# Kernel optimization log

Hardware: AMD Instinct MI355X
Metric: run time of the kernel (lower is better)

The kernel has to match this reference:

```python
import jax, jax.numpy as jnp
import numpy as np

N = 50000
IN_DIM = 1024
HID = 64
HEADS = 4
OUT_DIM = 128
NEG_SLOPE = 0.2


def setup_inputs() -> dict:
    key = jax.random.key(0)
    ks = jax.random.split(key, 10)
    x = jax.random.normal(ks[0], (N, IN_DIM), dtype=jnp.float32)
    edge_index = jax.random.randint(ks[1], (2, 800000), 0, N, dtype=jnp.int64)
    # GATConv 1: input_dim -> hidden_dim, heads=HEADS, concat=True
    W1 = jax.random.normal(ks[2], (IN_DIM, HEADS * HID), dtype=jnp.float32) * (1.0 / np.sqrt(IN_DIM))
    att_src1 = jax.random.normal(ks[3], (HEADS, HID), dtype=jnp.float32) * 0.1
    att_dst1 = jax.random.normal(ks[4], (HEADS, HID), dtype=jnp.float32) * 0.1
    b1 = jnp.zeros((HEADS * HID,), dtype=jnp.float32)
    # GATConv 2: hidden_dim*heads -> output_dim, heads=1, concat=False
    W2 = jax.random.normal(ks[5], (HEADS * HID, OUT_DIM), dtype=jnp.float32) * (1.0 / np.sqrt(HEADS * HID))
    att_src2 = jax.random.normal(ks[6], (1, OUT_DIM), dtype=jnp.float32) * 0.1
    att_dst2 = jax.random.normal(ks[7], (1, OUT_DIM), dtype=jnp.float32) * 0.1
    b2 = jnp.zeros((OUT_DIM,), dtype=jnp.float32)
    return {"x": x, "edge_index": edge_index, "W1": W1, "att_src1": att_src1,
            "att_dst1": att_dst1, "b1": b1, "W2": W2, "att_src2": att_src2,
            "att_dst2": att_dst2, "b2": b2}


def _gat_conv(x, src, dst, W, a_src, a_dst, b, heads, concat):
    # x: [N, F_in]; src/dst: [E'] (self-loops already included)
    n = x.shape[0]
    h = (x @ W).reshape(n, heads, -1)                 # [N, H, D]
    # per-node attention halves (PyG style)
    alpha_s = jnp.sum(h * a_src[None], axis=-1)       # [N, H]
    alpha_d = jnp.sum(h * a_dst[None], axis=-1)       # [N, H]
    e = jax.nn.leaky_relu(alpha_s[src] + alpha_d[dst], NEG_SLOPE)  # [E', H]
    # segment softmax over incoming edges of each destination node
    m = jax.ops.segment_max(e, dst, num_segments=n)   # [N, H]
    m = jnp.where(jnp.isfinite(m), m, 0.0)
    e = jnp.exp(e - m[dst])
    s = jax.ops.segment_sum(e, dst, num_segments=n)   # [N, H]
    alpha = e / (s[dst] + 1e-16)                      # [E', H]
    out = jax.ops.segment_sum(h[src] * alpha[:, :, None], dst, num_segments=n)  # [N, H, D]
    out = out.reshape(n, -1) if concat else out.mean(axis=1)
    return out + b


def reference(x, edge_index, W1, att_src1, att_dst1, b1, W2, att_src2, att_dst2, b2):
    n = x.shape[0]
    # PyG GATConv default: add self-loops
    loops = jnp.arange(n, dtype=edge_index.dtype)
    src = jnp.concatenate([edge_index[0], loops])
    dst = jnp.concatenate([edge_index[1], loops])
    # dropout layers are identity in eval mode
    h = _gat_conv(x, src, dst, W1, att_src1, att_dst1, b1, HEADS, concat=True)
    h = jax.nn.elu(h)
    out = _gat_conv(h, src, dst, W2, att_src2, att_dst2, b2, 1, concat=False)
    # F.normalize(p=2, dim=-1)
    norm = jnp.maximum(jnp.linalg.norm(out, axis=-1, keepdims=True), 1e-12)
    return out / norm
```

## Files before the change

kernel.cpp:

```cpp
#include <hip/hip_runtime.h>
#include <math.h>

#define NNODES 50000
#define E0 800000
#define ETOT 850000
#define IN_DIM 1024
#define HEADS 4
#define C1 256
#define C2 128
#define NEG_SLOPE 0.2f

typedef short bf16x8 __attribute__((ext_vector_type(8)));
typedef float f32x4 __attribute__((ext_vector_type(4)));
typedef unsigned short ushort_t;

__device__ __forceinline__ void edge_sd(const int* __restrict__ ei, int e, int& s, int& d) {
    if (e < E0) { s = ei[e]; d = ei[E0 + e]; }
    else        { s = e - E0; d = s; }
}

__device__ __forceinline__ ushort_t f2b(float f) {
    unsigned u = __float_as_uint(f);
    return (ushort_t)((u + 0x7fffu + ((u >> 16) & 1u)) >> 16);
}
__device__ __forceinline__ float bf2f(ushort_t u) {
    return __uint_as_float((unsigned)u << 16);
}
__device__ __forceinline__ float lrelu(float v) { return v > 0.f ? v : NEG_SLOPE * v; }

__device__ __forceinline__ bf16x8 cvt_bf8(float4 f0, float4 f1) {
    bf16x8 p;
    p[0] = f2b(f0.x); p[1] = f2b(f0.y); p[2] = f2b(f0.z); p[3] = f2b(f0.w);
    p[4] = f2b(f1.x); p[5] = f2b(f1.y); p[6] = f2b(f1.z); p[7] = f2b(f1.w);
    return p;
}

__global__ __launch_bounds__(256) void wtrans_kernel(const float* __restrict__ W,
                                                     ushort_t* __restrict__ WT,
                                                     int K, int N)
{
    int idx = blockIdx.x * 256 + threadIdx.x;
    if (idx >= K * N) return;
    int k = idx / N, n = idx % N;
    WT[((size_t)(k >> 3) * N + n) * 8 + (k & 7)] = f2b(W[idx]);
}

__global__ __launch_bounds__(256, 3) void gemm_fb(const float* __restrict__ A,
                                                  const ushort_t* __restrict__ Bblk,
                                                  ushort_t* __restrict__ Cb,
                                                  int M, int N, int K)
{
    __shared__ __align__(16) ushort_t As[32 * 64 * 8];

    const int tid  = threadIdx.x;
    const int lane = tid & 63;
    const int wid  = tid >> 6;
    const int wr   = wid >> 1, wc = wid & 1;
    const int rowBase = blockIdx.y * 64;
    const int colBase = blockIdx.x * 128;
    const int r0 = lane & 15;
    const int kh = lane >> 4;

    const int srow = tid >> 2;
    const int sq   = tid & 3;
    const float* aSrc = A + (size_t)min(rowBase + srow, M - 1) * K + sq * 64;
    ushort_t* aDst = As + (sq * 8) * 512 + srow * 8;

    const ushort_t* bBase = Bblk + ((size_t)kh * N + colBase + wc * 64 + r0) * 8;

    const ushort_t* aRd = As + kh * 512 + (wr * 32 + r0) * 8;

    f32x4 zero = {0.f, 0.f, 0.f, 0.f};
    f32x4 acc[2][4];
    #pragma unroll
    for (int i = 0; i < 2; ++i)
        #pragma unroll
        for (int j = 0; j < 4; ++j) acc[i][j] = zero;

    float4 st[16];
    #pragma unroll
    for (int i = 0; i < 16; ++i) st[i] = *(const float4*)(aSrc + i * 4);

    const int nstep = K >> 8;
    for (int s = 0; s < nstep; ++s) {
        __syncthreads();
        #pragma unroll
        for (int j = 0; j < 8; ++j)
            *(bf16x8*)(aDst + j * 512) = cvt_bf8(st[2 * j], st[2 * j + 1]);
        __syncthreads();

        if (s + 1 < nstep) {
            const float* nsrc = aSrc + (size_t)(s + 1) * 256;
            #pragma unroll
            for (int i = 0; i < 16; ++i) st[i] = *(const float4*)(nsrc + i * 4);
        }

        #pragma unroll
        for (int j = 0; j < 8; ++j) {
            const ushort_t* bit = bBase + ((size_t)(s * 32 + j * 4) * N) * 8;
            bf16x8 bF[4];
            #pragma unroll
            for (int fj = 0; fj < 4; ++fj)
                bF[fj] = *(const bf16x8*)(bit + (size_t)fj * 128);
            bf16x8 aF0 = *(const bf16x8*)(aRd + j * 2048);
            bf16x8 aF1 = *(const bf16x8*)(aRd + j * 2048 + 128);
            #pragma unroll
            for (int fj = 0; fj < 4; ++fj) {
                acc[0][fj] = __builtin_amdgcn_mfma_f32_16x16x32_bf16(aF0, bF[fj], acc[0][fj], 0, 0, 0);
                acc[1][fj] = __builtin_amdgcn_mfma_f32_16x16x32_bf16(aF1, bF[fj], acc[1][fj], 0, 0, 0);
            }
        }
    }

    #pragma unroll
    for (int fi = 0; fi < 2; ++fi) {
        int row0 = rowBase + wr * 32 + fi * 16 + kh * 4;
        #pragma unroll
        for (int i = 0; i < 4; ++i) {
            int row = row0 + i;
            if (row < M) {
                #pragma unroll
                for (int fj = 0; fj < 4; ++fj)
                    Cb[(size_t)row * N + colBase + wc * 64 + fj * 16 + r0] = f2b(acc[fi][fj][i]);
            }
        }
    }
}

__global__ __launch_bounds__(256, 4) void gemm_bb(const ushort_t* __restrict__ Ab,
                                                  const ushort_t* __restrict__ Bblk,
                                                  ushort_t* __restrict__ Cb,
                                                  int M, int N, int K)
{
    __shared__ __align__(16) ushort_t As[32 * 64 * 8];

    const int tid  = threadIdx.x;
    const int lane = tid & 63;
    const int wid  = tid >> 6;
    const int wr   = wid >> 1, wc = wid & 1;
    const int rowBase = blockIdx.y * 64;
    const int colBase = blockIdx.x * 128;
    const int r0 = lane & 15;
    const int kh = lane >> 4;

    const int srow = tid >> 2;
    const int sq   = tid & 3;
    const ushort_t* aSrc = Ab + (size_t)min(rowBase + srow, M - 1) * K + sq * 64;
    ushort_t* aDst = As + (sq * 8) * 512 + srow * 8;

    const ushort_t* bBase = Bblk + ((size_t)kh * N + colBase + wc * 64 + r0) * 8;
    const ushort_t* aRd = As + kh * 512 + (wr * 32 + r0) * 8;

    f32x4 zero = {0.f, 0.f, 0.f, 0.f};
    f32x4 acc[2][4];
    #pragma unroll
    for (int i = 0; i < 2; ++i)
        #pragma unroll
        for (int j = 0; j < 4; ++j) acc[i][j] = zero;

    bf16x8 st[8];
    #pragma unroll
    for (int j = 0; j < 8; ++j) st[j] = *(const bf16x8*)(aSrc + j * 8);

    const int nstep = K >> 8;
    for (int s = 0; s < nstep; ++s) {
        __syncthreads();
        #pragma unroll
        for (int j = 0; j < 8; ++j)
            *(bf16x8*)(aDst + j * 512) = st[j];
        __syncthreads();

        if (s + 1 < nstep) {
            const ushort_t* nsrc = aSrc + (size_t)(s + 1) * 256;
            #pragma unroll
            for (int j = 0; j < 8; ++j) st[j] = *(const bf16x8*)(nsrc + j * 8);
        }

        #pragma unroll
        for (int j = 0; j < 8; ++j) {
            const ushort_t* bit = bBase + ((size_t)(s * 32 + j * 4) * N) * 8;
            bf16x8 bF[4];
            #pragma unroll
            for (int fj = 0; fj < 4; ++fj)
                bF[fj] = *(const bf16x8*)(bit + (size_t)fj * 128);
            bf16x8 aF0 = *(const bf16x8*)(aRd + j * 2048);
            bf16x8 aF1 = *(const bf16x8*)(aRd + j * 2048 + 128);
            #pragma unroll
            for (int fj = 0; fj < 4; ++fj) {
                acc[0][fj] = __builtin_amdgcn_mfma_f32_16x16x32_bf16(aF0, bF[fj], acc[0][fj], 0, 0, 0);
                acc[1][fj] = __builtin_amdgcn_mfma_f32_16x16x32_bf16(aF1, bF[fj], acc[1][fj], 0, 0, 0);
            }
        }
    }

    #pragma unroll
    for (int fi = 0; fi < 2; ++fi) {
        int row0 = rowBase + wr * 32 + fi * 16 + kh * 4;
        #pragma unroll
        for (int i = 0; i < 4; ++i) {
            int row = row0 + i;
            if (row < M) {
                #pragma unroll
                for (int fj = 0; fj < 4; ++fj)
                    Cb[(size_t)row * N + colBase + wc * 64 + fj * 16 + r0] = f2b(acc[fi][fj][i]);
            }
        }
    }
}

__global__ __launch_bounds__(256) void alpha1_kernel(const ushort_t* __restrict__ h1b,
                                                     const float* __restrict__ asrc,
                                                     const float* __restrict__ adst,
                                                     float* __restrict__ out_s,
                                                     float* __restrict__ out_d)
{
    int n = blockIdx.x;
    int t = threadIdx.x;
    float h = bf2f(h1b[(size_t)n * C1 + t]);
    float s = h * asrc[t];
    float d = h * adst[t];
    #pragma unroll
    for (int off = 32; off > 0; off >>= 1) {
        s += __shfl_down(s, off);
        d += __shfl_down(d, off);
    }
    if ((t & 63) == 0) {
        out_s[n * HEADS + (t >> 6)] = s;
        out_d[n * HEADS + (t >> 6)] = d;
    }
}

__global__ __launch_bounds__(64) void alpha2_kernel(const ushort_t* __restrict__ h2b,
                                                    const float* __restrict__ asrc,
                                                    const float* __restrict__ adst,
                                                    float* __restrict__ out_s,
                                                    float* __restrict__ out_d)
{
    int n = blockIdx.x;
    int t = threadIdx.x;
    float a = bf2f(h2b[(size_t)n * C2 + t]);
    float b = bf2f(h2b[(size_t)n * C2 + t + 64]);
    float s = a * asrc[t] + b * asrc[t + 64];
    float d = a * adst[t] + b * adst[t + 64];
    #pragma unroll
    for (int off = 32; off > 0; off >>= 1) {
        s += __shfl_down(s, off);
        d += __shfl_down(d, off);
    }
    if (t == 0) { out_s[n] = s; out_d[n] = d; }
}

__global__ __launch_bounds__(256) void deg_kernel(const int* __restrict__ ei,
                                                  int* __restrict__ deg)
{
    int e = blockIdx.x * blockDim.x + threadIdx.x;
    if (e >= ETOT) return;
    int s, d; edge_sd(ei, e, s, d);
    atomicAdd(&deg[d], 1);
}

#define SCAN_T 1024
__global__ __launch_bounds__(SCAN_T) void scan_kernel(const int* __restrict__ deg,
                                                      int* __restrict__ rowptr)
{
    __shared__ int wsum[16];
    __shared__ int chunk_tot;
    __shared__ int carry_s;
    const int t = threadIdx.x, lane = t & 63, w = t >> 6;
    if (t == 0) carry_s = 0;
    __syncthreads();
    for (int base = 0; base < NNODES; base += SCAN_T * 4) {
        int idx = base + t * 4;
        int v0 = (idx + 0 < NNODES) ? deg[idx + 0] : 0;
        int v1 = (idx + 1 < NNODES) ? deg[idx + 1] : 0;
        int v2 = (idx + 2 < NNODES) ? deg[idx + 2] : 0;
        int v3 = (idx + 3 < NNODES) ? deg[idx + 3] : 0;
        int p0 = v0, p1 = p0 + v1, p2 = p1 + v2, p3 = p2 + v3;
        int incl = p3;
        #pragma unroll
        for (int off = 1; off < 64; off <<= 1) {
            int nb = __shfl_up(incl, off);
            if (lane >= off) incl += nb;
        }
        if (lane == 63) wsum[w] = incl;
        __syncthreads();
        if (w == 0 && lane < 16) {
            int ws = wsum[lane];
            int wincl = ws;
            #pragma unroll
            for (int off = 1; off < 16; off <<= 1) {
                int nb = __shfl_up(wincl, off);
                if (lane >= off) wincl += nb;
            }
            wsum[lane] = wincl - ws;
            if (lane == 15) chunk_tot = wincl;
        }
        __syncthreads();
        int carry = carry_s;
        int basev = carry + wsum[w] + (incl - p3);
        if (idx + 0 < NNODES) rowptr[idx + 0] = basev;
        if (idx + 1 < NNODES) rowptr[idx + 1] = basev + p0;
        if (idx + 2 < NNODES) rowptr[idx + 2] = basev + p1;
        if (idx + 3 < NNODES) rowptr[idx + 3] = basev + p2;
        __syncthreads();
        if (t == 0) carry_s = carry + chunk_tot;
        __syncthreads();
    }
    if (threadIdx.x == 0) rowptr[NNODES] = carry_s;
}

__global__ __launch_bounds__(256) void scatter_kernel(const int* __restrict__ ei,
                                                      int* __restrict__ cursor,
                                                      int* __restrict__ srcs)
{
    int e = blockIdx.x * blockDim.x + threadIdx.x;
    if (e >= ETOT) return;
    int s, d; edge_sd(ei, e, s, d);
    int pos = atomicAdd(&cursor[d], 1);
    srcs[pos] = s;
}

__global__ __launch_bounds__(256) void weights1_kernel(const int* __restrict__ rowptr,
                                                       const int* __restrict__ srcs,
                                                       const float4* __restrict__ as1,
                                                       const float4* __restrict__ ad1,
                                                       float4* __restrict__ wbuf)
{
    int d = blockIdx.x * 4 + (threadIdx.x >> 6);
    if (d >= NNODES) return;
    int lane = threadIdx.x & 63;
    int beg = rowptr[d], end = rowptr[d + 1];
    float4 adv = ad1[d];
    float m0 = -INFINITY, m1 = -INFINITY, m2 = -INFINITY, m3 = -INFINITY;
    for (int i = beg + lane; i < end; i += 64) {
        int s = srcs[i];
        float4 av = as1[s];
        m0 = fmaxf(m0, lrelu(av.x + adv.x));
        m1 = fmaxf(m1, lrelu(av.y + adv.y));
        m2 = fmaxf(m2, lrelu(av.z + adv.z));
        m3 = fmaxf(m3, lrelu(av.w + adv.w));
    }
    #pragma unroll
    for (int off = 32; off > 0; off >>= 1) {
        m0 = fmaxf(m0, __shfl_xor(m0, off));
        m1 = fmaxf(m1, __shfl_xor(m1, off));
        m2 = fmaxf(m2, __shfl_xor(m2, off));
        m3 = fmaxf(m3, __shfl_xor(m3, off));
    }
    float s0 = 0.f, s1 = 0.f, s2 = 0.f, s3 = 0.f;
    for (int i = beg + lane; i < end; i += 64) {
        int s = srcs[i];
        float4 av = as1[s];
        float w0 = expf(lrelu(av.x + adv.x) - m0);
        float w1 = expf(lrelu(av.y + adv.y) - m1);
        float w2 = expf(lrelu(av.z + adv.z) - m2);
        float w3 = expf(lrelu(av.w + adv.w) - m3);
        wbuf[i] = make_float4(w0, w1, w2, w3);
        s0 += w0; s1 += w1; s2 += w2; s3 += w3;
    }
    #pragma unroll
    for (int off = 32; off > 0; off >>= 1) {
        s0 += __shfl_xor(s0, off);
        s1 += __shfl_xor(s1, off);
        s2 += __shfl_xor(s2, off);
        s3 += __shfl_xor(s3, off);
    }
    float i0 = 1.f / (s0 + 1e-16f), i1 = 1.f / (s1 + 1e-16f);
    float i2 = 1.f / (s2 + 1e-16f), i3 = 1.f / (s3 + 1e-16f);
    for (int i = beg + lane; i < end; i += 64) {
        float4 wv = wbuf[i];
        wbuf[i] = make_float4(wv.x * i0, wv.y * i1, wv.z * i2, wv.w * i3);
    }
}

__global__ __launch_bounds__(256) void weights2_kernel(const int* __restrict__ rowptr,
                                                       const int* __restrict__ srcs,
                                                       const float* __restrict__ as2,
                                                       const float* __restrict__ ad2,
                                                       float* __restrict__ wbuf)
{
    int d = blockIdx.x * 4 + (threadIdx.x >> 6);
    if (d >= NNODES) return;
    int lane = threadIdx.x & 63;
    int beg = rowptr[d], end = rowptr[d + 1];
    float adv = ad2[d];
    float m = -INFINITY;
    for (int i = beg + lane; i < end; i += 64)
        m = fmaxf(m, lrelu(as2[srcs[i]] + adv));
    #pragma unroll
    for (int off = 32; off > 0; off >>= 1) m = fmaxf(m, __shfl_xor(m, off));
    float sm = 0.f;
    for (int i = beg + lane; i < end; i += 64) {
        float w = expf(lrelu(as2[srcs[i]] + adv) - m);
        wbuf[i] = w;
        sm += w;
    }
    #pragma unroll
    for (int off = 32; off > 0; off >>= 1) sm += __shfl_xor(sm, off);
    float inv = 1.f / (sm + 1e-16f);
    for (int i = beg + lane; i < end; i += 64) wbuf[i] *= inv;
}

__global__ __launch_bounds__(256) void aggr1_csr(const int* __restrict__ rowptr,
                                                 const int* __restrict__ srcs,
                                                 const ushort_t* __restrict__ h1b,
                                                 const float* __restrict__ wbuf,
                                                 const float* __restrict__ b1,
                                                 ushort_t* __restrict__ out)
{
    int d = blockIdx.x * 4 + (threadIdx.x >> 6);
    if (d >= NNODES) return;
    int lane = threadIdx.x & 63;
    int c0 = lane * 4;
    int head = lane >> 4;
    int beg = rowptr[d], end = rowptr[d + 1];
    float a0 = 0.f, a1 = 0.f, a2 = 0.f, a3 = 0.f;
    int i = beg;
    for (; i + 3 < end; i += 4) {
        int s0 = srcs[i], s1 = srcs[i + 1], s2 = srcs[i + 2], s3 = srcs[i + 3];
        float w0 = wbuf[i * 4 + head],     w1 = wbuf[i * 4 + 4 + head];
        float w2 = wbuf[i * 4 + 8 + head], w3 = wbuf[i * 4 + 12 + head];
        ushort4 v0 = *(const ushort4*)(h1b + (size_t)s0 * C1 + c0);
        ushort4 v1 = *(const ushort4*)(h1b + (size_t)s1 * C1 + c0);
        ushort4 v2 = *(const ushort4*)(h1b + (size_t)s2 * C1 + c0);
        ushort4 v3 = *(const ushort4*)(h1b + (size_t)s3 * C1 + c0);
        a0 = fmaf(w0, bf2f(v0.x), a0); a1 = fmaf(w0, bf2f(v0.y), a1);
        a2 = fmaf(w0, bf2f(v0.z), a2); a3 = fmaf(w0, bf2f(v0.w), a3);
        a0 = fmaf(w1, bf2f(v1.x), a0); a1 = fmaf(w1, bf2f(v1.y), a1);
        a2 = fmaf(w1, bf2f(v1.z), a2); a3 = fmaf(w1, bf2f(v1.w), a3);
        a0 = fmaf(w2, bf2f(v2.x), a0); a1 = fmaf(w2, bf2f(v2.y), a1);
        a2 = fmaf(w2, bf2f(v2.z), a2); a3 = fmaf(w2, bf2f(v2.w), a3);
        a0 = fmaf(w3, bf2f(v3.x), a0); a1 = fmaf(w3, bf2f(v3.y), a1);
        a2 = fmaf(w3, bf2f(v3.z), a2); a3 = fmaf(w3, bf2f(v3.w), a3);
    }
    for (; i < end; ++i) {
        int s0 = srcs[i];
        float w0 = wbuf[i * 4 + head];
        ushort4 v0 = *(const ushort4*)(h1b + (size_t)s0 * C1 + c0);
        a0 = fmaf(w0, bf2f(v0.x), a0); a1 = fmaf(w0, bf2f(v0.y), a1);
        a2 = fmaf(w0, bf2f(v0.z), a2); a3 = fmaf(w0, bf2f(v0.w), a3);
    }
    float4 bv = *(const float4*)(b1 + c0);
    float o0 = a0 + bv.x, o1 = a1 + bv.y, o2 = a2 + bv.z, o3 = a3 + bv.w;
    ushort4 r;
    r.x = f2b(o0 > 0.f ? o0 : (expf(o0) - 1.f));
    r.y = f2b(o1 > 0.f ? o1 : (expf(o1) - 1.f));
    r.z = f2b(o2 > 0.f ? o2 : (expf(o2) - 1.f));
    r.w = f2b(o3 > 0.f ? o3 : (expf(o3) - 1.f));
    *(ushort4*)(out + (size_t)d * C1 + c0) = r;
}

__global__ __launch_bounds__(256) void aggr2_csr(const int* __restrict__ rowptr,
                                                 const int* __restrict__ srcs,
                                                 const ushort_t* __restrict__ h2b,
                                                 const float* __restrict__ wbuf,
                                                 const float* __restrict__ b2,
                                                 float* __restrict__ out)
{
    int d = blockIdx.x * 4 + (threadIdx.x >> 6);
    if (d >= NNODES) return;
    int lane = threadIdx.x & 63;
    int c0 = lane * 2;
    int beg = rowptr[d], end = rowptr[d + 1];
    float a0 = 0.f, a1 = 0.f;
    int i = beg;
    for (; i + 3 < end; i += 4) {
        int s0 = srcs[i], s1 = srcs[i + 1], s2 = srcs[i + 2], s3 = srcs[i + 3];
        float w0 = wbuf[i], w1 = wbuf[i + 1], w2 = wbuf[i + 2], w3 = wbuf[i + 3];
        ushort2 v0 = *(const ushort2*)(h2b + (size_t)s0 * C2 + c0);
        ushort2 v1 = *(const ushort2*)(h2b + (size_t)s1 * C2 + c0);
        ushort2 v2 = *(const ushort2*)(h2b + (size_t)s2 * C2 + c0);
        ushort2 v3 = *(const ushort2*)(h2b + (size_t)s3 * C2 + c0);
        a0 = fmaf(w0, bf2f(v0.x), a0); a1 = fmaf(w0, bf2f(v0.y), a1);
        a0 = fmaf(w1, bf2f(v1.x), a0); a1 = fmaf(w1, bf2f(v1.y), a1);
        a0 = fmaf(w2, bf2f(v2.x), a0); a1 = fmaf(w2, bf2f(v2.y), a1);
        a0 = fmaf(w3, bf2f(v3.x), a0); a1 = fmaf(w3, bf2f(v3.y), a1);
    }
    for (; i < end; ++i) {
        float w0 = wbuf[i];
        ushort2 v0 = *(const ushort2*)(h2b + (size_t)srcs[i] * C2 + c0);
        a0 = fmaf(w0, bf2f(v0.x), a0); a1 = fmaf(w0, bf2f(v0.y), a1);
    }
    float2 bv = *(const float2*)(b2 + c0);
    float o0 = a0 + bv.x, o1 = a1 + bv.y;
    float sq = o0 * o0 + o1 * o1;
    #pragma unroll
    for (int off = 32; off > 0; off >>= 1) sq += __shfl_xor(sq, off);
    float inv = 1.0f / fmaxf(sqrtf(sq), 1e-12f);
    float2 r = make_float2(o0 * inv, o1 * inv);
    *(float2*)(out + (size_t)d * C2 + c0) = r;
}

extern "C" void kernel_launch(void* const* d_in, const int* in_sizes, int n_in,
                              void* d_out, int out_size, void* d_ws, size_t ws_size,
                              hipStream_t stream)
{
    const float* x     = (const float*)d_in[0];
    const int*   ei    = (const int*)d_in[1];
    const float* W1    = (const float*)d_in[2];
    const float* asrc1 = (const float*)d_in[3];
    const float* adst1 = (const float*)d_in[4];
    const float* b1    = (const float*)d_in[5];
    const float* W2    = (const float*)d_in[6];
    const float* asrc2 = (const float*)d_in[7];
    const float* adst2 = (const float*)d_in[8];
    const float* b2    = (const float*)d_in[9];
    float* out = (float*)d_out;

    char* ws = (char*)d_ws;
    size_t off = 0;
    auto alloc = [&](size_t nbytes) {
        void* p = ws + off;
        off += (nbytes + 15) & ~(size_t)15;
        return p;
    };
    ushort_t* h1b    = (ushort_t*)alloc((size_t)NNODES * C1 * 2);
    ushort_t* act1b  = (ushort_t*)alloc((size_t)NNODES * C1 * 2);
    ushort_t* h2b    = (ushort_t*)alloc((size_t)NNODES * C2 * 2);
    ushort_t* W1blk  = (ushort_t*)alloc((size_t)C1 * IN_DIM * 2);
    ushort_t* W2blk  = (ushort_t*)alloc((size_t)C2 * C1 * 2);
    float*    as1    = (float*)alloc((size_t)NNODES * HEADS * 4);
    float*    ad1    = (float*)alloc((size_t)NNODES * HEADS * 4);
    float*    as2    = (float*)alloc((size_t)NNODES * 4);
    float*    ad2    = (float*)alloc((size_t)NNODES * 4);
    float*    wbuf1  = (float*)alloc((size_t)ETOT * HEADS * 4);
    float*    wbuf2  = (float*)alloc((size_t)ETOT * 4);
    int*      deg    = (int*)alloc((size_t)NNODES * 4);
    int*      rowptr = (int*)alloc((size_t)(NNODES + 1) * 4);
    int*      cursor = (int*)alloc((size_t)(NNODES + 1) * 4);
    int*      srcs   = (int*)alloc((size_t)ETOT * 4);

    const int eb = (ETOT + 255) / 256;
    const int nb4 = (NNODES + 3) / 4;

    wtrans_kernel<<<(IN_DIM * C1 + 255) / 256, 256, 0, stream>>>(W1, W1blk, IN_DIM, C1);
    wtrans_kernel<<<(C1 * C2 + 255) / 256, 256, 0, stream>>>(W2, W2blk, C1, C2);

    hipMemsetAsync(deg, 0, (size_t)NNODES * 4, stream);
    deg_kernel<<<eb, 256, 0, stream>>>(ei, deg);
    scan_kernel<<<1, SCAN_T, 0, stream>>>(deg, rowptr);
    hipMemcpyAsync(cursor, rowptr, (size_t)(NNODES + 1) * 4, hipMemcpyDeviceToDevice, stream);
    scatter_kernel<<<eb, 256, 0, stream>>>(ei, cursor, srcs);

    dim3 g1(C1 / 128, (NNODES + 63) / 64);
    gemm_fb<<<g1, 256, 0, stream>>>(x, W1blk, h1b, NNODES, C1, IN_DIM);
    alpha1_kernel<<<NNODES, 256, 0, stream>>>(h1b, asrc1, adst1, as1, ad1);
    weights1_kernel<<<nb4, 256, 0, stream>>>(rowptr, srcs, (const float4*)as1,
                                             (const float4*)ad1, (float4*)wbuf1);
    aggr1_csr<<<nb4, 256, 0, stream>>>(rowptr, srcs, h1b, wbuf1, b1, act1b);

    dim3 g2(C2 / 128, (NNODES + 63) / 64);
    gemm_bb<<<g2, 256, 0, stream>>>(act1b, W2blk, h2b, NNODES, C2, C1);
    alpha2_kernel<<<NNODES, 64, 0, stream>>>(h2b, asrc2, adst2, as2, ad2);
    weights2_kernel<<<nb4, 256, 0, stream>>>(rowptr, srcs, as2, ad2, wbuf2);
    aggr2_csr<<<nb4, 256, 0, stream>>>(rowptr, srcs, h2b, wbuf2, b2, out);
}
```

Measured before the change: 484.7 us.

## Drop LDS staging in GEMMs; load A fragments directly from global per wave

Both GEMM kernels stop staging A tiles through shared memory with block-wide barriers. Each wave now loads its own 32-row A fragments straight from global memory in MFMA layout, double-buffered in registers, and covers a 32x64 output tile. The grid is remapped to 128-row by 64-column blocks with raised occupancy bounds. This removes the syncthreads and LDS traffic, but A rows are now reread once per 64-column tile instead of once per 128-column tile, and global loads are narrower per lane.

```diff
diff --git a/kernel.cpp b/kernel.cpp
--- a/kernel.cpp
+++ b/kernel.cpp
@@ -45,30 +45,23 @@
     WT[((size_t)(k >> 3) * N + n) * 8 + (k & 7)] = f2b(W[idx]);
 }
 
-__global__ __launch_bounds__(256, 3) void gemm_fb(const float* __restrict__ A,
+__global__ __launch_bounds__(256, 4) void gemm_fb(const float* __restrict__ A,
                                                   const ushort_t* __restrict__ Bblk,
                                                   ushort_t* __restrict__ Cb,
                                                   int M, int N, int K)
 {
-    __shared__ __align__(16) ushort_t As[32 * 64 * 8];
-
     const int tid  = threadIdx.x;
     const int lane = tid & 63;
     const int wid  = tid >> 6;
-    const int wr   = wid >> 1, wc = wid & 1;
-    const int rowBase = blockIdx.y * 64;
-    const int colBase = blockIdx.x * 128;
+    const int rowBase = blockIdx.x * 128 + wid * 32;
+    const int colBase = blockIdx.y * 64;
     const int r0 = lane & 15;
     const int kh = lane >> 4;
 
-    const int srow = tid >> 2;
-    const int sq   = tid & 3;
-    const float* aSrc = A + (size_t)min(rowBase + srow, M - 1) * K + sq * 64;
-    ushort_t* aDst = As + (sq * 8) * 512 + srow * 8;
-
-    const ushort_t* bBase = Bblk + ((size_t)kh * N + colBase + wc * 64 + r0) * 8;
-
-    const ushort_t* aRd = As + kh * 512 + (wr * 32 + r0) * 8;
+    const float* aP0 = A + (size_t)min(rowBase + r0,      M - 1) * K + kh * 8;
+    const float* aP1 = A + (size_t)min(rowBase + 16 + r0, M - 1) * K + kh * 8;
+    const ushort_t* bP = Bblk + ((size_t)kh * N + colBase + r0) * 8;
+    const size_t bStep = (size_t)4 * N * 8;
 
     f32x4 zero = {0.f, 0.f, 0.f, 0.f};
     f32x4 acc[2][4];
@@ -77,51 +70,59 @@
         #pragma unroll
         for (int j = 0; j < 4; ++j) acc[i][j] = zero;
 
-    float4 st[16];
-    #pragma unroll
-    for (int i = 0; i < 16; ++i) st[i] = *(const float4*)(aSrc + i * 4);
-
-    const int nstep = K >> 8;
-    for (int s = 0; s < nstep; ++s) {
-        __syncthreads();
-        #pragma unroll
-        for (int j = 0; j < 8; ++j)
-            *(bf16x8*)(aDst + j * 512) = cvt_bf8(st[2 * j], st[2 * j + 1]);
-        __syncthreads();
-
-        if (s + 1 < nstep) {
-            const float* nsrc = aSrc + (size_t)(s + 1) * 256;
-            #pragma unroll
-            for (int i = 0; i < 16; ++i) st[i] = *(const float4*)(nsrc + i * 4);
-        }
-
-        #pragma unroll
-        for (int j = 0; j < 8; ++j) {
-            const ushort_t* bit = bBase + ((size_t)(s * 32 + j * 4) * N) * 8;
+    float4 sa[4], sb[4];
+    sa[0] = *(const float4*)(aP0 + 0); sa[1] = *(const float4*)(aP0 + 4);
+    sa[2] = *(const float4*)(aP1 + 0); sa[3] = *(const float4*)(aP1 + 4);
+
+    const int nt = K >> 5;
+    for (int t = 0; t < nt; t += 2) {
+        {
+            const int kt1 = (t + 1) << 5;
+            sb[0] = *(const float4*)(aP0 + kt1 + 0); sb[1] = *(const float4*)(aP0 + kt1 + 4);
+            sb[2] = *(const float4*)(aP1 + kt1 + 0); sb[3] = *(const float4*)(aP1 + kt1 + 4);
+            const ushort_t* bb = bP + (size_t)t * bStep;
             bf16x8 bF[4];
             #pragma unroll
-            for (int fj = 0; fj < 4; ++fj)
-                bF[fj] = *(const bf16x8*)(bit + (size_t)fj * 128);
-            bf16x8 aF0 = *(const bf16x8*)(aRd + j * 2048);
-            bf16x8 aF1 = *(const bf16x8*)(aRd + j * 2048 + 128);
+            for (int fj = 0; fj < 4; ++fj) bF[fj] = *(const bf16x8*)(bb + fj * 128);
+            bf16x8 aF0 = cvt_bf8(sa[0], sa[1]);
+            bf16x8 aF1 = cvt_bf8(sa[2], sa[3]);
             #pragma unroll
             for (int fj = 0; fj < 4; ++fj) {
                 acc[0][fj] = __builtin_amdgcn_mfma_f32_16x16x32_bf16(aF0, bF[fj], acc[0][fj], 0, 0, 0);
                 acc[1][fj] = __builtin_amdgcn_mfma_f32_16x16x32_bf16(aF1, bF[fj], acc[1][fj], 0, 0, 0);
             }
         }
+        {
+            const bool has2 = (t + 2) < nt;
+            if (has2) {
+                const int kt2 = (t + 2) << 5;
+                sa[0] = *(const float4*)(aP0 + kt2 + 0); sa[1] = *(const float4*)(aP0 + kt2 + 4);
+                sa[2] = *(const float4*)(aP1 + kt2 + 0); sa[3] = *(const float4*)(aP1 + kt2 + 4);
+            }
+            const ushort_t* bb = bP + (size_t)(t + 1) * bStep;
+            bf16x8 bF[4];
+            #pragma unroll
+            for (int fj = 0; fj < 4; ++fj) bF[fj] = *(const bf16x8*)(bb + fj * 128);
+            bf16x8 aF0 = cvt_bf8(sb[0], sb[1]);
+            bf16x8 aF1 = cvt_bf8(sb[2], sb[3]);
+            #pragma unroll
+            for (int fj = 0; fj < 4; ++fj) {
+                acc[0][fj] = __builtin_amdgcn_mfma_f32_16x16x32_bf16(aF0, bF[fj], acc[0][fj], 0, 0, 0);
+                acc[1][fj] = __builtin_amdgcn_mfma_f32_16x16x32_bf16(aF1, bF[fj], acc[1][fj], 0, 0, 0);
+            }
+        }
     }
 
     #pragma unroll
     for (int fi = 0; fi < 2; ++fi) {
-        int row0 = rowBase + wr * 32 + fi * 16 + kh * 4;
+        int row0 = rowBase + fi * 16 + kh * 4;
         #pragma unroll
         for (int i = 0; i < 4; ++i) {
             int row = row0 + i;
             if (row < M) {
                 #pragma unroll
                 for (int fj = 0; fj < 4; ++fj)
-                    Cb[(size_t)row * N + colBase + wc * 64 + fj * 16 + r0] = f2b(acc[fi][fj][i]);
+                    Cb[(size_t)row * N + colBase + fj * 16 + r0] = f2b(acc[fi][fj][i]);
             }
         }
     }
@@ -132,24 +133,18 @@
                                                   ushort_t* __restrict__ Cb,
                                                   int M, int N, int K)
 {
-    __shared__ __align__(16) ushort_t As[32 * 64 * 8];
-
     const int tid  = threadIdx.x;
     const int lane = tid & 63;
     const int wid  = tid >> 6;
-    const int wr   = wid >> 1, wc = wid & 1;
-    const int rowBase = blockIdx.y * 64;
-    const int colBase = blockIdx.x * 128;
+    const int rowBase = blockIdx.x * 128 + wid * 32;
+    const int colBase = blockIdx.y * 64;
     const int r0 = lane & 15;
     const int kh = lane >> 4;
 
-    const int srow = tid >> 2;
-    const int sq   = tid & 3;
-    const ushort_t* aSrc = Ab + (size_t)min(rowBase + srow, M - 1) * K + sq * 64;
-    ushort_t* aDst = As + (sq * 8) * 512 + srow * 8;
-
-    const ushort_t* bBase = Bblk + ((size_t)kh * N + colBase + wc * 64 + r0) * 8;
-    const ushort_t* aRd = As + kh * 512 + (wr * 32 + r0) * 8;
+    const ushort_t* aP0 = Ab + (size_t)min(rowBase + r0,      M - 1) * K + kh * 8;
+    const ushort_t* aP1 = Ab + (size_t)min(rowBase + 16 + r0, M - 1) * K + kh * 8;
+    const ushort_t* bP = Bblk + ((size_t)kh * N + colBase + r0) * 8;
+    const size_t bStep = (size_t)4 * N * 8;
 
     f32x4 zero = {0.f, 0.f, 0.f, 0.f};
     f32x4 acc[2][4];
@@ -158,51 +153,52 @@
         #pragma unroll
         for (int j = 0; j < 4; ++j) acc[i][j] = zero;
 
-    bf16x8 st[8];
-    #pragma unroll
-    for (int j = 0; j < 8; ++j) st[j] = *(const bf16x8*)(aSrc + j * 8);
-
-    const int nstep = K >> 8;
-    for (int s = 0; s < nstep; ++s) {
-        __syncthreads();
-        #pragma unroll
-        for (int j = 0; j < 8; ++j)
-            *(bf16x8*)(aDst + j * 512) = st[j];
-        __syncthreads();
-
-        if (s + 1 < nstep) {
-            const ushort_t* nsrc = aSrc + (size_t)(s + 1) * 256;
-            #pragma unroll
-            for (int j = 0; j < 8; ++j) st[j] = *(const bf16x8*)(nsrc + j * 8);
-        }
-
-        #pragma unroll
-        for (int j = 0; j < 8; ++j) {
-            const ushort_t* bit = bBase + ((size_t)(s * 32 + j * 4) * N) * 8;
+    bf16x8 sa0, sa1, sb0, sb1;
+    sa0 = *(const bf16x8*)(aP0); sa1 = *(const bf16x8*)(aP1);
+
+    const int nt = K >> 5;
+    for (int t = 0; t < nt; t += 2) {
+        {
+            const int kt1 = (t + 1) << 5;
+            sb0 = *(const bf16x8*)(aP0 + kt1); sb1 = *(const bf16x8*)(aP1 + kt1);
+            const ushort_t* bb = bP + (size_t)t * bStep;
             bf16x8 bF[4];
             #pragma unroll
-            for (int fj = 0; fj < 4; ++fj)
-                bF[fj] = *(const bf16x8*)(bit + (size_t)fj * 128);
-            bf16x8 aF0 = *(const bf16x8*)(aRd + j * 2048);
-            bf16x8 aF1 = *(const bf16x8*)(aRd + j * 2048 + 128);
+            for (int fj = 0; fj < 4; ++fj) bF[fj] = *(const bf16x8*)(bb + fj * 128);
             #pragma unroll
             for (int fj = 0; fj < 4; ++fj) {
-                acc[0][fj] = __builtin_amdgcn_mfma_f32_16x16x32_bf16(aF0, bF[fj], acc[0][fj], 0, 0, 0);
-                acc[1][fj] = __builtin_amdgcn_mfma_f32_16x16x32_bf16(aF1, bF[fj], acc[1][fj], 0, 0, 0);
+                acc[0][fj] = __builtin_amdgcn_mfma_f32_16x16x32_bf16(sa0, bF[fj], acc[0][fj], 0, 0, 0);
+                acc[1][fj] = __builtin_amdgcn_mfma_f32_16x16x32_bf16(sa1, bF[fj], acc[1][fj], 0, 0, 0);
+            }
+        }
+        {
+            const bool has2 = (t + 2) < nt;
+            if (has2) {
+                const int kt2 = (t + 2) << 5;
+                sa0 = *(const bf16x8*)(aP0 + kt2); sa1 = *(const bf16x8*)(aP1 + kt2);
+            }
+            const ushort_t* bb = bP + (size_t)(t + 1) * bStep;
+            bf16x8 bF[4];
+            #pragma unroll
+            for (int fj = 0; fj < 4; ++fj) bF[fj] = *(const bf16x8*)(bb + fj * 128);
+            #pragma unroll
+            for (int fj = 0; fj < 4; ++fj) {
+                acc[0][fj] = __builtin_amdgcn_mfma_f32_16x16x32_bf16(sb0, bF[fj], acc[0][fj], 0, 0, 0);
+                acc[1][fj] = __builtin_amdgcn_mfma_f32_16x16x32_bf16(sb1, bF[fj], acc[1][fj], 0, 0, 0);
             }
         }
     }
 
     #pragma unroll
     for (int fi = 0; fi < 2; ++fi) {
-        int row0 = rowBase + wr * 32 + fi * 16 + kh * 4;
+        int row0 = rowBase + fi * 16 + kh * 4;
         #pragma unroll
         for (int i = 0; i < 4; ++i) {
             int row = row0 + i;
             if (row < M) {
                 #pragma unroll
                 for (int fj = 0; fj < 4; ++fj)
-                    Cb[(size_t)row * N + colBase + wc * 64 + fj * 16 + r0] = f2b(acc[fi][fj][i]);
+                    Cb[(size_t)row * N + colBase + fj * 16 + r0] = f2b(acc[fi][fj][i]);
             }
         }
     }
@@ -532,6 +528,7 @@
 
     const int eb = (ETOT + 255) / 256;
     const int nb4 = (NNODES + 3) / 4;
+    const int rb = (NNODES + 127) / 128;
 
     wtrans_kernel<<<(IN_DIM * C1 + 255) / 256, 256, 0, stream>>>(W1, W1blk, IN_DIM, C1);
     wtrans_kernel<<<(C1 * C2 + 255) / 256, 256, 0, stream>>>(W2, W2blk, C1, C2);
@@ -542,14 +539,14 @@
     hipMemcpyAsync(cursor, rowptr, (size_t)(NNODES + 1) * 4, hipMemcpyDeviceToDevice, stream);
     scatter_kernel<<<eb, 256, 0, stream>>>(ei, cursor, srcs);
 
-    dim3 g1(C1 / 128, (NNODES + 63) / 64);
+    dim3 g1(rb, C1 / 64);
     gemm_fb<<<g1, 256, 0, stream>>>(x, W1blk, h1b, NNODES, C1, IN_DIM);
     alpha1_kernel<<<NNODES, 256, 0, stream>>>(h1b, asrc1, adst1, as1, ad1);
     weights1_kernel<<<nb4, 256, 0, stream>>>(rowptr, srcs, (const float4*)as1,
                                              (const float4*)ad1, (float4*)wbuf1);
     aggr1_csr<<<nb4, 256, 0, stream>>>(rowptr, srcs, h1b, wbuf1, b1, act1b);
 
-    dim3 g2(C2 / 128, (NNODES + 63) / 64);
+    dim3 g2(rb, C2 / 64);
     gemm_bb<<<g2, 256, 0, stream>>>(act1b, W2blk, h2b, NNODES, C2, C1);
     alpha2_kernel<<<NNODES, 64, 0, stream>>>(h2b, asrc2, adst2, as2, ad2);
     weights2_kernel<<<nb4, 256, 0, stream>>>(rowptr, srcs, as2, ad2, wbuf2);
```

After: 480.3 us. About the same (-0.9%).
